# Optimization experiments

Measured on AMD Instinct MI355X. Metric: run time of the kernel, lower is better.

Reference implementation:

```python
import jax, jax.numpy as jnp
import numpy as np

B, N = 262144, 32
NEG = -1e4  # acts as -inf: exp(NEG) == 0 in fp32, clean gradients (softmax weight 0)


def setup_inputs() -> dict:
    key = jax.random.key(0)
    k1, k2, k3 = jax.random.split(key, 3)
    scores = jax.random.normal(k1, (B, N), dtype=jnp.float32)
    ranks = jax.random.randint(k2, (B, N), 0, 32, dtype=jnp.int64)
    mask = jax.random.randint(k3, (B, N), 0, 2, dtype=jnp.int32).astype(bool)
    return {"scores": scores, "ranks": ranks, "mask": mask}


def reference(scores, ranks, mask):
    # n valid (non-padded) items per row
    n = jnp.sum(~mask, axis=1)                              # [B]
    # sort each row by rank, pushing padded entries to the end (stable sort,
    # matching per-row argsort over the valid subset in the original)
    sort_key = jnp.where(mask, N + 1, ranks)                # [B, N]
    order = jnp.argsort(sort_key, axis=1)                   # jnp argsort is stable
    s_sorted = jnp.take_along_axis(scores, order, axis=1)   # [B, N]

    pos = jnp.arange(N)
    valid = pos[None, :] < n[:, None]                       # first n slots hold valid scores
    s_m = jnp.where(valid, s_sorted, NEG)                   # padded -> effectively -inf

    # reverse cumulative logsumexp: rev_lse[k] = logsumexp(s_sorted[k:n])
    rev_lse = jax.lax.cumlogsumexp(s_m, axis=1, reverse=True)

    # original sums k = 0 .. n-2 of -(s_k - logsumexp(s_{k:}))
    term_mask = pos[None, :] < (n[:, None] - 1)
    per_row = -jnp.sum(jnp.where(term_mask, s_m - rev_lse, 0.0), axis=1)  # [B]

    use = n >= 2                                            # rows with < 2 valid are skipped
    per_row = jnp.where(use, per_row / jnp.maximum(n, 1).astype(per_row.dtype), 0.0)
    n_valid = jnp.sum(use)
    return jnp.sum(per_row) / jnp.maximum(n_valid, 1).astype(per_row.dtype)
```

## Files before the change

kernel.cpp:

```cpp
#include <hip/hip_runtime.h>
#include <cstdint>

#define TPB 256
#define LOG2E 1.4426950408889634f
#define LN2   0.69314718055994531f
#define RS    36
#define VALID_LIM (1024u << 16)

__global__ __launch_bounds__(TPB, 4)
void pl_main(const float* __restrict__ scores,
             const int* __restrict__ ranks,
             const int* __restrict__ mask,
             float* __restrict__ partials,
             int B)
{
    const int tid = threadIdx.x;

    __shared__ unsigned pb[TPB * RS];

    const size_t tile4 = (size_t)blockIdx.x * (TPB * 8);
    const size_t tot4  = (size_t)B * 8;

    const float4* sp = reinterpret_cast<const float4*>(scores) + tile4;
    const int4*   rp = reinterpret_cast<const int4*>(ranks)   + tile4;
    const int4*   mp = reinterpret_cast<const int4*>(mask)    + tile4;

    #pragma unroll
    for (int i = 0; i < 8; ++i) {
        const int f = i * TPB + tid;
        if (tile4 + f < tot4) {
            const float4 sv = sp[f];
            const int4   rv = rp[f];
            const int4   qv = mp[f];
            const int rowL = f >> 3;
            const int j0   = (f & 7) * 4;

            uint4 w;
            {
                const float e = __builtin_amdgcn_exp2f(sv.x * LOG2E);
                const unsigned b = __builtin_bit_cast(unsigned, e);
                const unsigned b16 = (b + 0x7FFFu + ((b >> 16) & 1u)) >> 16;
                w.x = ((unsigned)((qv.x << 10) + (rv.x << 5) + (j0 + 0)) << 16) | b16;
            }
            {
                const float e = __builtin_amdgcn_exp2f(sv.y * LOG2E);
                const unsigned b = __builtin_bit_cast(unsigned, e);
                const unsigned b16 = (b + 0x7FFFu + ((b >> 16) & 1u)) >> 16;
                w.y = ((unsigned)((qv.y << 10) + (rv.y << 5) + (j0 + 1)) << 16) | b16;
            }
            {
                const float e = __builtin_amdgcn_exp2f(sv.z * LOG2E);
                const unsigned b = __builtin_bit_cast(unsigned, e);
                const unsigned b16 = (b + 0x7FFFu + ((b >> 16) & 1u)) >> 16;
                w.z = ((unsigned)((qv.z << 10) + (rv.z << 5) + (j0 + 2)) << 16) | b16;
            }
            {
                const float e = __builtin_amdgcn_exp2f(sv.w * LOG2E);
                const unsigned b = __builtin_bit_cast(unsigned, e);
                const unsigned b16 = (b + 0x7FFFu + ((b >> 16) & 1u)) >> 16;
                w.w = ((unsigned)((qv.w << 10) + (rv.w << 5) + (j0 + 3)) << 16) | b16;
            }
            *reinterpret_cast<uint4*>(&pb[rowL * RS + j0]) = w;
        }
    }
    __syncthreads();

    float per_row = 0.0f, cnt = 0.0f;
    const int row = blockIdx.x * TPB + tid;

    if (row < B) {
        unsigned U[32];
        #pragma unroll
        for (int c = 0; c < 8; ++c) {
            const uint4 v = *reinterpret_cast<const uint4*>(&pb[tid * RS + c * 4]);
            U[c*4+0] = v.x; U[c*4+1] = v.y; U[c*4+2] = v.z; U[c*4+3] = v.w;
        }

        #pragma unroll
        for (int kk = 2; kk <= 32; kk <<= 1) {
            #pragma unroll
            for (int jj = kk >> 1; jj > 0; jj >>= 1) {
                #pragma unroll
                for (int i = 0; i < 32; ++i) {
                    const int l = i ^ jj;
                    if (l > i) {
                        const unsigned a = U[i], b = U[l];
                        const unsigned mn = a < b ? a : b;
                        const unsigned mh = a < b ? b : a;
                        if ((i & kk) == 0) { U[i] = mn; U[l] = mh; }
                        else               { U[i] = mh; U[l] = mn; }
                    }
                }
            }
        }

        int   n = 0;
        float t = 0.0f, lsum = 0.0f;
        #pragma unroll
        for (int g = 7; g >= 0; --g) {
            float pT = 1.0f, pE = 1.0f;
            #pragma unroll
            for (int q = 3; q >= 0; --q) {
                const int p = 4*g + q;
                const bool v = (U[p] < VALID_LIM);
                const float e = __builtin_bit_cast(float, U[p] << 16);
                n  += v ? 1 : 0;
                t  += v ? e : 0.0f;
                pT *= v ? t : 1.0f;
                pE *= v ? e : 1.0f;
            }
            lsum += __builtin_amdgcn_logf(pT) - __builtin_amdgcn_logf(pE);
        }

        if (n >= 2) {
            per_row = (LN2 * lsum) / (float)n;
            cnt = 1.0f;
        }
    }

    #pragma unroll
    for (int d = 32; d >= 1; d >>= 1) {
        per_row += __shfl_xor(per_row, d, 64);
        cnt     += __shfl_xor(cnt,     d, 64);
    }
    __shared__ float rbuf[8];
    if ((tid & 63) == 0) {
        rbuf[(tid >> 6)]     = per_row;
        rbuf[4 + (tid >> 6)] = cnt;
    }
    __syncthreads();
    if (tid == 0) {
        partials[2*blockIdx.x]     = (rbuf[0] + rbuf[1]) + (rbuf[2] + rbuf[3]);
        partials[2*blockIdx.x + 1] = (rbuf[4] + rbuf[5]) + (rbuf[6] + rbuf[7]);
    }
}

__global__ __launch_bounds__(256)
void pl_final(const float* __restrict__ partials, int nb, float* __restrict__ out)
{
    const int tid = threadIdx.x;
    float s = 0.0f, c = 0.0f;
    for (int i = tid; i < nb; i += 256) {
        s += partials[2*i];
        c += partials[2*i + 1];
    }
    #pragma unroll
    for (int d = 32; d >= 1; d >>= 1) {
        s += __shfl_xor(s, d, 64);
        c += __shfl_xor(c, d, 64);
    }
    __shared__ float sb[8];
    if ((tid & 63) == 0) {
        sb[tid >> 6]       = s;
        sb[4 + (tid >> 6)] = c;
    }
    __syncthreads();
    if (tid == 0) {
        const float S = sb[0] + sb[1] + sb[2] + sb[3];
        const float C = sb[4] + sb[5] + sb[6] + sb[7];
        out[0] = S / fmaxf(C, 1.0f);
    }
}

extern "C" void kernel_launch(void* const* d_in, const int* in_sizes, int n_in,
                              void* d_out, int out_size, void* d_ws, size_t ws_size,
                              hipStream_t stream)
{
    const float* scores = (const float*)d_in[0];
    const int*   ranks  = (const int*)d_in[1];
    const int*   mask   = (const int*)d_in[2];

    const int B  = in_sizes[0] / 32;
    const int nb = (B + TPB - 1) / TPB;

    float* partials = (float*)d_ws;

    pl_main<<<nb, TPB, 0, stream>>>(scores, ranks, mask, partials, B);
    pl_final<<<1, 256, 0, stream>>>(partials, nb, (float*)d_out);
}
```

Before: 28.69 us.

## Load rows directly per thread and fuse final reduction via last-block atomic

Each thread now reads its own row's 32 scores, ranks and mask straight from global memory into registers, replacing the coalesced cooperative load staged through a shared-memory transpose buffer. The separate finalize kernel is removed. The last block to finish, found with an atomic counter, performs the cross-block reduction, and a memset now resets the counter before each launch. This saves the LDS traffic, a barrier and a kernel launch, but per-thread strided 16-byte loads are less coalesced and the memset adds a stream operation.

```diff
diff --git a/kernel.cpp b/kernel.cpp
--- a/kernel.cpp
+++ b/kernel.cpp
@@ -4,76 +4,46 @@
 #define TPB 256
 #define LOG2E 1.4426950408889634f
 #define LN2   0.69314718055994531f
-#define RS    36
 #define VALID_LIM (1024u << 16)
 
+__device__ __forceinline__ unsigned pack_e(float s, int key)
+{
+    const float e = __builtin_amdgcn_exp2f(s * LOG2E);
+    const unsigned b = __builtin_bit_cast(unsigned, e);
+    const unsigned b16 = (b + 0x7FFFu + ((b >> 16) & 1u)) >> 16;
+    return ((unsigned)key << 16) | b16;
+}
+
 __global__ __launch_bounds__(TPB, 4)
-void pl_main(const float* __restrict__ scores,
-             const int* __restrict__ ranks,
-             const int* __restrict__ mask,
-             float* __restrict__ partials,
-             int B)
+void pl_fused(const float* __restrict__ scores,
+              const int* __restrict__ ranks,
+              const int* __restrict__ mask,
+              float* __restrict__ partials,
+              unsigned* __restrict__ counter,
+              float* __restrict__ out,
+              int B, int nb)
 {
     const int tid = threadIdx.x;
-
-    __shared__ unsigned pb[TPB * RS];
-
-    const size_t tile4 = (size_t)blockIdx.x * (TPB * 8);
-    const size_t tot4  = (size_t)B * 8;
-
-    const float4* sp = reinterpret_cast<const float4*>(scores) + tile4;
-    const int4*   rp = reinterpret_cast<const int4*>(ranks)   + tile4;
-    const int4*   mp = reinterpret_cast<const int4*>(mask)    + tile4;
-
-    #pragma unroll
-    for (int i = 0; i < 8; ++i) {
-        const int f = i * TPB + tid;
-        if (tile4 + f < tot4) {
-            const float4 sv = sp[f];
-            const int4   rv = rp[f];
-            const int4   qv = mp[f];
-            const int rowL = f >> 3;
-            const int j0   = (f & 7) * 4;
-
-            uint4 w;
-            {
-                const float e = __builtin_amdgcn_exp2f(sv.x * LOG2E);
-                const unsigned b = __builtin_bit_cast(unsigned, e);
-                const unsigned b16 = (b + 0x7FFFu + ((b >> 16) & 1u)) >> 16;
-                w.x = ((unsigned)((qv.x << 10) + (rv.x << 5) + (j0 + 0)) << 16) | b16;
-            }
-            {
-                const float e = __builtin_amdgcn_exp2f(sv.y * LOG2E);
-                const unsigned b = __builtin_bit_cast(unsigned, e);
-                const unsigned b16 = (b + 0x7FFFu + ((b >> 16) & 1u)) >> 16;
-                w.y = ((unsigned)((qv.y << 10) + (rv.y << 5) + (j0 + 1)) << 16) | b16;
-            }
-            {
-                const float e = __builtin_amdgcn_exp2f(sv.z * LOG2E);
-                const unsigned b = __builtin_bit_cast(unsigned, e);
-                const unsigned b16 = (b + 0x7FFFu + ((b >> 16) & 1u)) >> 16;
-                w.z = ((unsigned)((qv.z << 10) + (rv.z << 5) + (j0 + 2)) << 16) | b16;
-            }
-            {
-                const float e = __builtin_amdgcn_exp2f(sv.w * LOG2E);
-                const unsigned b = __builtin_bit_cast(unsigned, e);
-                const unsigned b16 = (b + 0x7FFFu + ((b >> 16) & 1u)) >> 16;
-                w.w = ((unsigned)((qv.w << 10) + (rv.w << 5) + (j0 + 3)) << 16) | b16;
-            }
-            *reinterpret_cast<uint4*>(&pb[rowL * RS + j0]) = w;
-        }
-    }
-    __syncthreads();
+    const int row = blockIdx.x * TPB + tid;
 
     float per_row = 0.0f, cnt = 0.0f;
-    const int row = blockIdx.x * TPB + tid;
 
     if (row < B) {
+        const float4* sp = reinterpret_cast<const float4*>(scores) + (size_t)row * 8;
+        const int4*   rp = reinterpret_cast<const int4*>(ranks)  + (size_t)row * 8;
+        const int4*   mp = reinterpret_cast<const int4*>(mask)   + (size_t)row * 8;
+
         unsigned U[32];
         #pragma unroll
         for (int c = 0; c < 8; ++c) {
-            const uint4 v = *reinterpret_cast<const uint4*>(&pb[tid * RS + c * 4]);
-            U[c*4+0] = v.x; U[c*4+1] = v.y; U[c*4+2] = v.z; U[c*4+3] = v.w;
+            const float4 sv = sp[c];
+            const int4   rv = rp[c];
+            const int4   qv = mp[c];
+            const int j = c * 4;
+            U[j+0] = pack_e(sv.x, (qv.x << 10) + (rv.x << 5) + (j+0));
+            U[j+1] = pack_e(sv.y, (qv.y << 10) + (rv.y << 5) + (j+1));
+            U[j+2] = pack_e(sv.z, (qv.z << 10) + (rv.z << 5) + (j+2));
+            U[j+3] = pack_e(sv.w, (qv.w << 10) + (rv.w << 5) + (j+3));
         }
 
         #pragma unroll
@@ -124,6 +94,7 @@
         cnt     += __shfl_xor(cnt,     d, 64);
     }
     __shared__ float rbuf[8];
+    __shared__ bool  amLast;
     if ((tid & 63) == 0) {
         rbuf[(tid >> 6)]     = per_row;
         rbuf[4 + (tid >> 6)] = cnt;
@@ -132,33 +103,34 @@
     if (tid == 0) {
         partials[2*blockIdx.x]     = (rbuf[0] + rbuf[1]) + (rbuf[2] + rbuf[3]);
         partials[2*blockIdx.x + 1] = (rbuf[4] + rbuf[5]) + (rbuf[6] + rbuf[7]);
-    }
-}
-
-__global__ __launch_bounds__(256)
-void pl_final(const float* __restrict__ partials, int nb, float* __restrict__ out)
-{
-    const int tid = threadIdx.x;
-    float s = 0.0f, c = 0.0f;
-    for (int i = tid; i < nb; i += 256) {
-        s += partials[2*i];
-        c += partials[2*i + 1];
-    }
-    #pragma unroll
-    for (int d = 32; d >= 1; d >>= 1) {
-        s += __shfl_xor(s, d, 64);
-        c += __shfl_xor(c, d, 64);
-    }
-    __shared__ float sb[8];
-    if ((tid & 63) == 0) {
-        sb[tid >> 6]       = s;
-        sb[4 + (tid >> 6)] = c;
+        __threadfence();
+        const unsigned prev = atomicAdd(counter, 1u);
+        amLast = (prev == (unsigned)(nb - 1));
     }
     __syncthreads();
-    if (tid == 0) {
-        const float S = sb[0] + sb[1] + sb[2] + sb[3];
-        const float C = sb[4] + sb[5] + sb[6] + sb[7];
-        out[0] = S / fmaxf(C, 1.0f);
+
+    if (amLast) {
+        __threadfence();
+        float s = 0.0f, c = 0.0f;
+        for (int i = tid; i < nb; i += TPB) {
+            s += partials[2*i];
+            c += partials[2*i + 1];
+        }
+        #pragma unroll
+        for (int d = 32; d >= 1; d >>= 1) {
+            s += __shfl_xor(s, d, 64);
+            c += __shfl_xor(c, d, 64);
+        }
+        if ((tid & 63) == 0) {
+            rbuf[(tid >> 6)]     = s;
+            rbuf[4 + (tid >> 6)] = c;
+        }
+        __syncthreads();
+        if (tid == 0) {
+            const float S = (rbuf[0] + rbuf[1]) + (rbuf[2] + rbuf[3]);
+            const float C = (rbuf[4] + rbuf[5]) + (rbuf[6] + rbuf[7]);
+            out[0] = S / fmaxf(C, 1.0f);
+        }
     }
 }
 
@@ -173,8 +145,10 @@
     const int B  = in_sizes[0] / 32;
     const int nb = (B + TPB - 1) / TPB;
 
-    float* partials = (float*)d_ws;
+    unsigned* counter  = (unsigned*)d_ws;
+    float*    partials = (float*)((char*)d_ws + 16);
 
-    pl_main<<<nb, TPB, 0, stream>>>(scores, ranks, mask, partials, B);
-    pl_final<<<1, 256, 0, stream>>>(partials, nb, (float*)d_out);
+    hipMemsetAsync(counter, 0, 4, stream);
+    pl_fused<<<nb, TPB, 0, stream>>>(scores, ranks, mask, partials, counter,
+                                     (float*)d_out, B, nb);
 }
```

Result: slower. 69.37 us (+141.8%).

## Make each wavefront process its own 64 rows without block barriers

Applied to the files above, without the earlier changes.

Each 64-lane wavefront now stages, sorts and reduces its own 64 rows in a private LDS slice, so both __syncthreads barriers and the cross-wave shared reduction are gone. Each wave writes its own float2 partial, and the final kernel sums twice as many partials. The LDS row stride changes from 36 with 128-bit accesses to 33 with scalar accesses, trading vector LDS ops for fewer bank conflicts. Block size drops to 128 and the occupancy hint is removed.

```diff
diff --git a/kernel.cpp b/kernel.cpp
--- a/kernel.cpp
+++ b/kernel.cpp
@@ -1,80 +1,67 @@
 #include <hip/hip_runtime.h>
 #include <cstdint>
 
-#define TPB 256
+#define TPB 128
 #define LOG2E 1.4426950408889634f
 #define LN2   0.69314718055994531f
-#define RS    36
+#define RSTR  33
 #define VALID_LIM (1024u << 16)
 
-__global__ __launch_bounds__(TPB, 4)
+__device__ __forceinline__ unsigned pack1(float s, int q, int r, int j)
+{
+    const float e = __builtin_amdgcn_exp2f(s * LOG2E);
+    const unsigned b = __builtin_bit_cast(unsigned, e);
+    const unsigned b16 = (b + 0x7FFFu + ((b >> 16) & 1u)) >> 16;
+    return ((unsigned)((q << 10) + (r << 5) + j) << 16) | b16;
+}
+
+__global__ __launch_bounds__(TPB)
 void pl_main(const float* __restrict__ scores,
              const int* __restrict__ ranks,
              const int* __restrict__ mask,
-             float* __restrict__ partials,
+             float2* __restrict__ partials,
              int B)
 {
-    const int tid = threadIdx.x;
+    const int tid  = threadIdx.x;
+    const int lane = tid & 63;
+    const int wid  = tid >> 6;
 
-    __shared__ unsigned pb[TPB * RS];
+    __shared__ unsigned pb[TPB / 64][64 * RSTR];
+    unsigned* pw = pb[wid];
 
-    const size_t tile4 = (size_t)blockIdx.x * (TPB * 8);
-    const size_t tot4  = (size_t)B * 8;
+    const int    rowBase = blockIdx.x * TPB + wid * 64;
+    const size_t base4   = (size_t)rowBase * 8;
+    const size_t tot4    = (size_t)B * 8;
 
-    const float4* sp = reinterpret_cast<const float4*>(scores) + tile4;
-    const int4*   rp = reinterpret_cast<const int4*>(ranks)   + tile4;
-    const int4*   mp = reinterpret_cast<const int4*>(mask)    + tile4;
+    const float4* sp = reinterpret_cast<const float4*>(scores) + base4;
+    const int4*   rp = reinterpret_cast<const int4*>(ranks)   + base4;
+    const int4*   mp = reinterpret_cast<const int4*>(mask)    + base4;
 
+    const bool full = (base4 + 8 * 64 <= tot4);
     #pragma unroll
     for (int i = 0; i < 8; ++i) {
-        const int f = i * TPB + tid;
-        if (tile4 + f < tot4) {
+        const int f = i * 64 + lane;
+        if (full || base4 + f < tot4) {
             const float4 sv = sp[f];
             const int4   rv = rp[f];
             const int4   qv = mp[f];
-            const int rowL = f >> 3;
-            const int j0   = (f & 7) * 4;
-
-            uint4 w;
-            {
-                const float e = __builtin_amdgcn_exp2f(sv.x * LOG2E);
-                const unsigned b = __builtin_bit_cast(unsigned, e);
-                const unsigned b16 = (b + 0x7FFFu + ((b >> 16) & 1u)) >> 16;
-                w.x = ((unsigned)((qv.x << 10) + (rv.x << 5) + (j0 + 0)) << 16) | b16;
-            }
-            {
-                const float e = __builtin_amdgcn_exp2f(sv.y * LOG2E);
-                const unsigned b = __builtin_bit_cast(unsigned, e);
-                const unsigned b16 = (b + 0x7FFFu + ((b >> 16) & 1u)) >> 16;
-                w.y = ((unsigned)((qv.y << 10) + (rv.y << 5) + (j0 + 1)) << 16) | b16;
-            }
-            {
-                const float e = __builtin_amdgcn_exp2f(sv.z * LOG2E);
-                const unsigned b = __builtin_bit_cast(unsigned, e);
-                const unsigned b16 = (b + 0x7FFFu + ((b >> 16) & 1u)) >> 16;
-                w.z = ((unsigned)((qv.z << 10) + (rv.z << 5) + (j0 + 2)) << 16) | b16;
-            }
-            {
-                const float e = __builtin_amdgcn_exp2f(sv.w * LOG2E);
-                const unsigned b = __builtin_bit_cast(unsigned, e);
-                const unsigned b16 = (b + 0x7FFFu + ((b >> 16) & 1u)) >> 16;
-                w.w = ((unsigned)((qv.w << 10) + (rv.w << 5) + (j0 + 3)) << 16) | b16;
-            }
-            *reinterpret_cast<uint4*>(&pb[rowL * RS + j0]) = w;
+            const int r  = f >> 3;
+            const int j0 = (f & 7) << 2;
+            pw[r * RSTR + j0 + 0] = pack1(sv.x, qv.x, rv.x, j0 + 0);
+            pw[r * RSTR + j0 + 1] = pack1(sv.y, qv.y, rv.y, j0 + 1);
+            pw[r * RSTR + j0 + 2] = pack1(sv.z, qv.z, rv.z, j0 + 2);
+            pw[r * RSTR + j0 + 3] = pack1(sv.w, qv.w, rv.w, j0 + 3);
         }
     }
-    __syncthreads();
 
     float per_row = 0.0f, cnt = 0.0f;
-    const int row = blockIdx.x * TPB + tid;
+    const int row = rowBase + lane;
 
     if (row < B) {
         unsigned U[32];
         #pragma unroll
-        for (int c = 0; c < 8; ++c) {
-            const uint4 v = *reinterpret_cast<const uint4*>(&pb[tid * RS + c * 4]);
-            U[c*4+0] = v.x; U[c*4+1] = v.y; U[c*4+2] = v.z; U[c*4+3] = v.w;
-        }
+        for (int j = 0; j < 32; ++j)
+            U[j] = pw[lane * RSTR + j];
 
         #pragma unroll
         for (int kk = 2; kk <= 32; kk <<= 1) {
@@ -123,26 +110,19 @@
         per_row += __shfl_xor(per_row, d, 64);
         cnt     += __shfl_xor(cnt,     d, 64);
     }
-    __shared__ float rbuf[8];
-    if ((tid & 63) == 0) {
-        rbuf[(tid >> 6)]     = per_row;
-        rbuf[4 + (tid >> 6)] = cnt;
-    }
-    __syncthreads();
-    if (tid == 0) {
-        partials[2*blockIdx.x]     = (rbuf[0] + rbuf[1]) + (rbuf[2] + rbuf[3]);
-        partials[2*blockIdx.x + 1] = (rbuf[4] + rbuf[5]) + (rbuf[6] + rbuf[7]);
-    }
+    if (lane == 0)
+        partials[blockIdx.x * (TPB / 64) + wid] = make_float2(per_row, cnt);
 }
 
 __global__ __launch_bounds__(256)
-void pl_final(const float* __restrict__ partials, int nb, float* __restrict__ out)
+void pl_final(const float2* __restrict__ partials, int np, float* __restrict__ out)
 {
     const int tid = threadIdx.x;
     float s = 0.0f, c = 0.0f;
-    for (int i = tid; i < nb; i += 256) {
-        s += partials[2*i];
-        c += partials[2*i + 1];
+    for (int i = tid; i < np; i += 256) {
+        const float2 v = partials[i];
+        s += v.x;
+        c += v.y;
     }
     #pragma unroll
     for (int d = 32; d >= 1; d >>= 1) {
@@ -156,8 +136,8 @@
     }
     __syncthreads();
     if (tid == 0) {
-        const float S = sb[0] + sb[1] + sb[2] + sb[3];
-        const float C = sb[4] + sb[5] + sb[6] + sb[7];
+        const float S = (sb[0] + sb[1]) + (sb[2] + sb[3]);
+        const float C = (sb[4] + sb[5]) + (sb[6] + sb[7]);
         out[0] = S / fmaxf(C, 1.0f);
     }
 }
@@ -172,9 +152,10 @@
 
     const int B  = in_sizes[0] / 32;
     const int nb = (B + TPB - 1) / TPB;
+    const int np = nb * (TPB / 64);
 
-    float* partials = (float*)d_ws;
+    float2* partials = (float2*)d_ws;
 
     pl_main<<<nb, TPB, 0, stream>>>(scores, ranks, mask, partials, B);
-    pl_final<<<1, 256, 0, stream>>>(partials, nb, (float*)d_out);
+    pl_final<<<1, 256, 0, stream>>>(partials, np, (float*)d_out);
 }
```

Result: slower. 30.86 us (+7.6%).
